# Optimization experiments

Measured on AMD Instinct MI355X. Metric: run time of the kernel, lower is better.

## Reference

```python
import jax, jax.numpy as jnp
import numpy as np

Z_DIM, Y_DIM, X_DIM, N_ACT = 32, 16, 64, 4
TINY_H, HEAD_H = 64, 32
INNER_STEPS, SUP_STEPS = 2, 2
BATCH = 524288


def setup_inputs() -> dict:
    key = jax.random.key(0)
    ks = jax.random.split(key, 12)
    s = lambda k, shp, fan_in: jax.random.normal(k, shp, jnp.float32) * (1.0 / np.sqrt(fan_in))
    return {
        "state": jax.random.normal(ks[0], (BATCH, X_DIM), jnp.float32),
        "prev_action": jax.random.randint(ks[1], (BATCH, 1), 0, N_ACT, jnp.int64),
        "z0": jax.random.normal(ks[2], (1, 1, Z_DIM), jnp.float32) * 0.1,
        # TinyNetwork: Linear(112 -> 64), Linear(64 -> 32); weights stored [out, in]
        "Wt1": s(ks[3], (TINY_H, Z_DIM + X_DIM + Y_DIM), Z_DIM + X_DIM + Y_DIM),
        "bt1": jnp.zeros((TINY_H,), jnp.float32),
        "Wt2": s(ks[4], (Z_DIM, TINY_H), TINY_H),
        "bt2": jnp.zeros((Z_DIM,), jnp.float32),
        # OutputHead: Linear(48 -> 32), Linear(32 -> 4)
        "Wh1": s(ks[5], (HEAD_H, Z_DIM + Y_DIM), Z_DIM + Y_DIM),
        "bh1": jnp.zeros((HEAD_H,), jnp.float32),
        "Wh2": s(ks[6], (N_ACT, HEAD_H), HEAD_H),
        "bh2": jnp.zeros((N_ACT,), jnp.float32),
        # action embedding table [n_actions, y_dim]
        "emb": jax.random.normal(ks[7], (N_ACT, Y_DIM), jnp.float32),
    }


def reference(state, prev_action, z0, Wt1, bt1, Wt2, bt2, Wh1, bh1, Wh2, bh2, emb):
    B = state.shape[0]
    x = state[:, None, :]                      # [B, 1, x_dim]
    y = emb[prev_action]                       # [B, 1, y_dim]
    z = jnp.broadcast_to(z0, (B, 1, Z_DIM))    # [B, 1, z_dim]

    def tiny(z, x, y):
        inp = jnp.concatenate([z, x, y], axis=-1)           # [B,1,112]
        h = jax.nn.relu(inp @ Wt1.T + bt1)                  # [B,1,64]
        return h @ Wt2.T + bt2                              # [B,1,32]

    def head(z, y):
        inp = jnp.concatenate([z, y], axis=-1)              # [B,1,48]
        h = jax.nn.relu(inp @ Wh1.T + bh1)                  # [B,1,32]
        return h @ Wh2.T + bh2                              # [B,1,4]

    logits = None
    for _ in range(SUP_STEPS):
        for _ in range(INNER_STEPS):
            z = tiny(z, x, y)
        logits = head(z, y)
        probs = jax.nn.softmax(logits, axis=-1)             # [B,1,4]
        y = probs @ emb                                     # [B,1,16]
    return logits[:, 0, :]                                  # squeeze seq dim
```

## Files before the change

### kernel.cpp

```cpp
#include <hip/hip_runtime.h>
#include <hip/hip_bf16.h>

typedef __attribute__((ext_vector_type(8))) short bf16x8;
typedef __attribute__((ext_vector_type(4))) float f32x4;

#define MFMA16(A,B,C) __builtin_amdgcn_mfma_f32_16x16x32_bf16((A),(B),(C),0,0,0)

static __device__ __forceinline__ f32x4 ld4(const float* p){
  return *(const f32x4*)p;
}
static __device__ __forceinline__ unsigned pk2(float a, float b){
  unsigned r;
  asm("v_cvt_pk_bf16_f32 %0, %1, %2" : "=v"(r) : "v"(a), "v"(b));
  return r;
}
static __device__ __forceinline__ bf16x8 mk8(float a,float b,float c,float d,
                                             float e,float f,float g,float h){
  union { bf16x8 v; unsigned u[4]; } r;
  r.u[0]=pk2(a,b); r.u[1]=pk2(c,d); r.u[2]=pk2(e,f); r.u[3]=pk2(g,h);
  return r.v;
}
static __device__ __forceinline__ bf16x8 mk8v(f32x4 a, f32x4 b){
  return mk8(a[0],a[1],a[2],a[3],b[0],b[1],b[2],b[3]);
}
static __device__ __forceinline__ bf16x8 mk8r(f32x4 a, f32x4 b){
  return mk8(fmaxf(a[0],0.f),fmaxf(a[1],0.f),fmaxf(a[2],0.f),fmaxf(a[3],0.f),
             fmaxf(b[0],0.f),fmaxf(b[1],0.f),fmaxf(b[2],0.f),fmaxf(b[3],0.f));
}
static __device__ __forceinline__ bf16x8 zero8(){
  bf16x8 v;
  #pragma unroll
  for(int i=0;i<8;++i) v[i]=0;
  return v;
}
static __device__ __forceinline__ void keepa(bf16x8& v){ asm("" : "+a"(v)); }
static __device__ __forceinline__ void keepaf(f32x4& v){ asm("" : "+a"(v)); }

__global__ __launch_bounds__(256, 1) void trm_mfma(
    const float* __restrict__ state, const int* __restrict__ pact,
    const float* __restrict__ z0,
    const float* __restrict__ Wt1, const float* __restrict__ bt1,
    const float* __restrict__ Wt2, const float* __restrict__ bt2,
    const float* __restrict__ Wh1, const float* __restrict__ bh1,
    const float* __restrict__ Wh2, const float* __restrict__ bh2,
    const float* __restrict__ emb, float* __restrict__ out,
    int ntiles, int wstride)
{
  const int lane = threadIdx.x & 63;
  const int wid  = blockIdx.x * (blockDim.x >> 6) + (threadIdx.x >> 6);
  const int r16  = lane & 15;
  const int hi   = lane >> 4;
  const int he   = hi & 1;

  bf16x8 wt1f[4][4];
  #pragma unroll
  for (int m=0;m<4;++m){
    const float* w = Wt1 + (m*16 + r16)*112;
    wt1f[m][0] = mk8v(ld4(w + hi*4),       ld4(w + 16 + hi*4));
    wt1f[m][1] = mk8v(ld4(w + 32 + hi*8),  ld4(w + 36 + hi*8));
    wt1f[m][2] = mk8v(ld4(w + 64 + hi*8),  ld4(w + 68 + hi*8));
    bf16x8 yfrag = mk8v(ld4(w + 96 + he*8), ld4(w + 100 + he*8));
    if (hi >= 2) yfrag = zero8();
    wt1f[m][3] = yfrag;
    keepa(wt1f[m][0]); keepa(wt1f[m][1]); keepa(wt1f[m][2]); keepa(wt1f[m][3]);
  }
  bf16x8 wt2f[2][2];
  #pragma unroll
  for (int m=0;m<2;++m){
    const float* w = Wt2 + (m*16 + r16)*64;
    wt2f[m][0] = mk8v(ld4(w + hi*4),      ld4(w + 16 + hi*4));
    wt2f[m][1] = mk8v(ld4(w + 32 + hi*4), ld4(w + 48 + hi*4));
    keepa(wt2f[m][0]); keepa(wt2f[m][1]);
  }
  bf16x8 wh1f[2][2];
  #pragma unroll
  for (int m=0;m<2;++m){
    const float* w = Wh1 + (m*16 + r16)*48;
    wh1f[m][0] = mk8v(ld4(w + hi*4), ld4(w + 16 + hi*4));
    bf16x8 yfrag = mk8v(ld4(w + 32 + he*8), ld4(w + 36 + he*8));
    if (hi >= 2) yfrag = zero8();
    wh1f[m][1] = yfrag;
    keepa(wh1f[m][0]); keepa(wh1f[m][1]);
  }
  bf16x8 wh2f;
  {
    const float* w = Wh2 + ((r16 < 4) ? r16 : 0)*32;
    bf16x8 t = mk8v(ld4(w + hi*4), ld4(w + 16 + hi*4));
    if (r16 >= 4) t = zero8();
    wh2f = t;
    keepa(wh2f);
  }
  f32x4 bt1r[4], bt2r[2], bh1r[2], bh2r;
  #pragma unroll
  for (int m=0;m<4;++m){ bt1r[m] = ld4(bt1 + m*16 + hi*4); keepaf(bt1r[m]); }
  #pragma unroll
  for (int m=0;m<2;++m){ bt2r[m] = ld4(bt2 + m*16 + hi*4); keepaf(bt2r[m]); }
  #pragma unroll
  for (int m=0;m<2;++m){ bh1r[m] = ld4(bh1 + m*16 + hi*4); keepaf(bh1r[m]); }
  {
    f32x4 t = ld4(bh2);
    float msk = (hi == 0) ? 1.f : 0.f;
    bh2r = t * msk;
    keepaf(bh2r);
  }
  bf16x8 z0f = mk8v(ld4(z0 + hi*4), ld4(z0 + 16 + hi*4));
  keepa(z0f);

  int t = wid;
  f32x4 cx0, cx1, cx2, cx3; int cact;
  {
    const int col = t*16 + r16;
    const float* xr = state + (size_t)col*64;
    cx0 = ld4(xr + hi*8);      cx1 = ld4(xr + hi*8 + 4);
    cx2 = ld4(xr + 32 + hi*8); cx3 = ld4(xr + 36 + hi*8);
    cact = pact[col];
  }

  #pragma unroll 1
  for (; t < ntiles; t += wstride){
    const int col = t*16 + r16;
    bf16x8 xf0 = mk8v(cx0, cx1);
    bf16x8 xf1 = mk8v(cx2, cx3);
    bf16x8 yf;
    {
      const float* er = emb + cact*16 + he*8;
      yf = mk8v(ld4(er), ld4(er + 4));
      if (hi >= 2) yf = zero8();
    }

    const int tn = t + wstride;
    if (tn < ntiles){
      const int coln = tn*16 + r16;
      const float* xrn = state + (size_t)coln*64;
      cx0 = ld4(xrn + hi*8);      cx1 = ld4(xrn + hi*8 + 4);
      cx2 = ld4(xrn + 32 + hi*8); cx3 = ld4(xrn + 36 + hi*8);
      cact = pact[coln];
    }

    bf16x8 zf = z0f;
    f32x4 lgv;

    #pragma unroll
    for (int s=0;s<2;++s){
      #pragma unroll
      for (int itr=0; itr<2; ++itr){
        f32x4 c0 = MFMA16(wt1f[0][0], zf, bt1r[0]);
        f32x4 c1 = MFMA16(wt1f[1][0], zf, bt1r[1]);
        f32x4 c2 = MFMA16(wt1f[2][0], zf, bt1r[2]);
        f32x4 c3 = MFMA16(wt1f[3][0], zf, bt1r[3]);
        c0=MFMA16(wt1f[0][1], xf0, c0); c1=MFMA16(wt1f[1][1], xf0, c1);
        c2=MFMA16(wt1f[2][1], xf0, c2); c3=MFMA16(wt1f[3][1], xf0, c3);
        c0=MFMA16(wt1f[0][2], xf1, c0); c1=MFMA16(wt1f[1][2], xf1, c1);
        c2=MFMA16(wt1f[2][2], xf1, c2); c3=MFMA16(wt1f[3][2], xf1, c3);
        c0=MFMA16(wt1f[0][3], yf,  c0); c1=MFMA16(wt1f[1][3], yf,  c1);
        c2=MFMA16(wt1f[2][3], yf,  c2); c3=MFMA16(wt1f[3][3], yf,  c3);
        bf16x8 h0 = mk8r(c0, c1);
        bf16x8 h1 = mk8r(c2, c3);
        f32x4 d0 = MFMA16(wt2f[0][0], h0, bt2r[0]);
        f32x4 d1 = MFMA16(wt2f[1][0], h0, bt2r[1]);
        d0=MFMA16(wt2f[0][1], h1, d0);
        d1=MFMA16(wt2f[1][1], h1, d1);
        zf = mk8v(d0, d1);
      }
      f32x4 g0 = MFMA16(wh1f[0][0], zf, bh1r[0]);
      f32x4 g1 = MFMA16(wh1f[1][0], zf, bh1r[1]);
      g0=MFMA16(wh1f[0][1], yf, g0);
      g1=MFMA16(wh1f[1][1], yf, g1);
      bf16x8 hh = mk8r(g0, g1);
      f32x4 cl = MFMA16(wh2f, hh, bh2r);
      lgv = cl;
      if (s == 0){
        float l0 = __shfl(cl[0], r16), l1 = __shfl(cl[1], r16);
        float l2 = __shfl(cl[2], r16), l3 = __shfl(cl[3], r16);
        float mx = fmaxf(fmaxf(l0,l1), fmaxf(l2,l3));
        float p0=__expf(l0-mx), p1=__expf(l1-mx);
        float p2=__expf(l2-mx), p3=__expf(l3-mx);
        float inv = 1.f/(p0+p1+p2+p3);
        p0*=inv; p1*=inv; p2*=inv; p3*=inv;
        const float* eb = emb + he*8;
        f32x4 ya = ld4(eb)*p0      + ld4(eb+16)*p1 +
                   ld4(eb+32)*p2   + ld4(eb+48)*p3;
        f32x4 yb = ld4(eb+4)*p0    + ld4(eb+20)*p1 +
                   ld4(eb+36)*p2   + ld4(eb+52)*p3;
        yf = mk8v(ya, yb);
        if (hi >= 2) yf = zero8();
      }
    }
    if (hi == 0) *(f32x4*)(out + (size_t)col*4) = lgv;
  }
}

extern "C" void kernel_launch(void* const* d_in, const int* in_sizes, int n_in,
                              void* d_out, int out_size, void* d_ws, size_t ws_size,
                              hipStream_t stream) {
  const float* state = (const float*)d_in[0];
  const int*   pact  = (const int*)  d_in[1];
  const float* z0    = (const float*)d_in[2];
  const float* Wt1   = (const float*)d_in[3];
  const float* bt1   = (const float*)d_in[4];
  const float* Wt2   = (const float*)d_in[5];
  const float* bt2   = (const float*)d_in[6];
  const float* Wh1   = (const float*)d_in[7];
  const float* bh1   = (const float*)d_in[8];
  const float* Wh2   = (const float*)d_in[9];
  const float* bh2   = (const float*)d_in[10];
  const float* emb   = (const float*)d_in[11];
  float* out = (float*)d_out;

  const int B = in_sizes[0] / 64;
  const int ntiles = B / 16;
  const int blocks = 1024;
  const int wstride = blocks * 4;
  trm_mfma<<<blocks, 256, 0, stream>>>(state, pact, z0, Wt1, bt1, Wt2, bt2,
                                       Wh1, bh1, Wh2, bh2, emb, out,
                                       ntiles, wstride);
}
```

Measured before the change: 63.22 us.

## Fold biases into MFMA via constant-one input lane, stage emb in LDS

Folds bt2 into the downstream biases (bt1' = bt1 + Wt1_z·bt2, bh1' = bh1 + Wh1_z·bt2, z0 shifted by -bt2) and injects those biases through an extra constant-one entry in the padded y fragment. MFMAs can then accumulate from a shared zero register instead of bias registers, which frees registers. The embedding table is staged in shared memory, launch bounds allow two blocks per CU, and the grid is halved. Folding the biases in bf16 adds rounding error, and fewer blocks may reduce latency hiding.

```diff
diff --git a/kernel.cpp b/kernel.cpp
--- a/kernel.cpp
+++ b/kernel.cpp
@@ -33,10 +33,17 @@
   for(int i=0;i<8;++i) v[i]=0;
   return v;
 }
+static __device__ __forceinline__ bf16x8 one8(){
+  bf16x8 v = zero8();
+  v[0] = (short)0x3F80;
+  return v;
+}
 static __device__ __forceinline__ void keepa(bf16x8& v){ asm("" : "+a"(v)); }
 static __device__ __forceinline__ void keepaf(f32x4& v){ asm("" : "+a"(v)); }
-
-__global__ __launch_bounds__(256, 1) void trm_mfma(
+static __device__ __forceinline__ void keepv(bf16x8& v){ asm("" : "+v"(v)); }
+static __device__ __forceinline__ void keepvf(f32x4& v){ asm("" : "+v"(v)); }
+
+__global__ __launch_bounds__(256, 2) void trm_mfma(
     const float* __restrict__ state, const int* __restrict__ pact,
     const float* __restrict__ z0,
     const float* __restrict__ Wt1, const float* __restrict__ bt1,
@@ -46,12 +53,38 @@
     const float* __restrict__ emb, float* __restrict__ out,
     int ntiles, int wstride)
 {
+  __shared__ __align__(16) float ef[64];
   const int lane = threadIdx.x & 63;
   const int wid  = blockIdx.x * (blockDim.x >> 6) + (threadIdx.x >> 6);
   const int r16  = lane & 15;
   const int hi   = lane >> 4;
   const int he   = hi & 1;
 
+  if (threadIdx.x < 64) ef[threadIdx.x] = emb[threadIdx.x];
+  __syncthreads();
+
+  f32x4 b2[8];
+  #pragma unroll
+  for (int q=0;q<8;++q) b2[q] = ld4(bt2 + q*4);
+  float bt1p[4];
+  #pragma unroll
+  for (int m=0;m<4;++m){
+    const float* w = Wt1 + (m*16 + r16)*112;
+    f32x4 s = b2[0]*ld4(w);
+    #pragma unroll
+    for (int q=1;q<8;++q) s += b2[q]*ld4(w + q*4);
+    bt1p[m] = bt1[m*16 + r16] + s[0]+s[1]+s[2]+s[3];
+  }
+  float bh1p[2];
+  #pragma unroll
+  for (int m=0;m<2;++m){
+    const float* w = Wh1 + (m*16 + r16)*48;
+    f32x4 s = b2[0]*ld4(w);
+    #pragma unroll
+    for (int q=1;q<8;++q) s += b2[q]*ld4(w + q*4);
+    bh1p[m] = bh1[m*16 + r16] + s[0]+s[1]+s[2]+s[3];
+  }
+
   bf16x8 wt1f[4][4];
   #pragma unroll
   for (int m=0;m<4;++m){
@@ -59,8 +92,10 @@
     wt1f[m][0] = mk8v(ld4(w + hi*4),       ld4(w + 16 + hi*4));
     wt1f[m][1] = mk8v(ld4(w + 32 + hi*8),  ld4(w + 36 + hi*8));
     wt1f[m][2] = mk8v(ld4(w + 64 + hi*8),  ld4(w + 68 + hi*8));
-    bf16x8 yfrag = mk8v(ld4(w + 96 + he*8), ld4(w + 100 + he*8));
-    if (hi >= 2) yfrag = zero8();
+    bf16x8 yfrag;
+    if (hi < 2)       yfrag = mk8v(ld4(w + 96 + hi*8), ld4(w + 100 + hi*8));
+    else if (hi == 2) yfrag = mk8(bt1p[m],0.f,0.f,0.f,0.f,0.f,0.f,0.f);
+    else              yfrag = zero8();
     wt1f[m][3] = yfrag;
     keepa(wt1f[m][0]); keepa(wt1f[m][1]); keepa(wt1f[m][2]); keepa(wt1f[m][3]);
   }
@@ -77,8 +112,10 @@
   for (int m=0;m<2;++m){
     const float* w = Wh1 + (m*16 + r16)*48;
     wh1f[m][0] = mk8v(ld4(w + hi*4), ld4(w + 16 + hi*4));
-    bf16x8 yfrag = mk8v(ld4(w + 32 + he*8), ld4(w + 36 + he*8));
-    if (hi >= 2) yfrag = zero8();
+    bf16x8 yfrag;
+    if (hi < 2)       yfrag = mk8v(ld4(w + 32 + hi*8), ld4(w + 36 + hi*8));
+    else if (hi == 2) yfrag = mk8(bh1p[m],0.f,0.f,0.f,0.f,0.f,0.f,0.f);
+    else              yfrag = zero8();
     wh1f[m][1] = yfrag;
     keepa(wh1f[m][0]); keepa(wh1f[m][1]);
   }
@@ -90,21 +127,22 @@
     wh2f = t;
     keepa(wh2f);
   }
-  f32x4 bt1r[4], bt2r[2], bh1r[2], bh2r;
-  #pragma unroll
-  for (int m=0;m<4;++m){ bt1r[m] = ld4(bt1 + m*16 + hi*4); keepaf(bt1r[m]); }
-  #pragma unroll
-  for (int m=0;m<2;++m){ bt2r[m] = ld4(bt2 + m*16 + hi*4); keepaf(bt2r[m]); }
-  #pragma unroll
-  for (int m=0;m<2;++m){ bh1r[m] = ld4(bh1 + m*16 + hi*4); keepaf(bh1r[m]); }
+  f32x4 bh2r;
   {
     f32x4 t = ld4(bh2);
     float msk = (hi == 0) ? 1.f : 0.f;
     bh2r = t * msk;
     keepaf(bh2r);
   }
-  bf16x8 z0f = mk8v(ld4(z0 + hi*4), ld4(z0 + 16 + hi*4));
-  keepa(z0f);
+  f32x4 zero4 = {0.f, 0.f, 0.f, 0.f};
+  keepvf(zero4);
+  bf16x8 z0f;
+  {
+    f32x4 za = ld4(z0 + hi*4)      - ld4(bt2 + hi*4);
+    f32x4 zb = ld4(z0 + 16 + hi*4) - ld4(bt2 + 16 + hi*4);
+    z0f = mk8v(za, zb);
+    keepv(z0f);
+  }
 
   int t = wid;
   f32x4 cx0, cx1, cx2, cx3; int cact;
@@ -123,9 +161,10 @@
     bf16x8 xf1 = mk8v(cx2, cx3);
     bf16x8 yf;
     {
-      const float* er = emb + cact*16 + he*8;
+      const float* er = ef + cact*16 + he*8;
       yf = mk8v(ld4(er), ld4(er + 4));
-      if (hi >= 2) yf = zero8();
+      if (hi == 2) yf = one8();
+      if (hi == 3) yf = zero8();
     }
 
     const int tn = t + wstride;
@@ -144,10 +183,10 @@
     for (int s=0;s<2;++s){
       #pragma unroll
       for (int itr=0; itr<2; ++itr){
-        f32x4 c0 = MFMA16(wt1f[0][0], zf, bt1r[0]);
-        f32x4 c1 = MFMA16(wt1f[1][0], zf, bt1r[1]);
-        f32x4 c2 = MFMA16(wt1f[2][0], zf, bt1r[2]);
-        f32x4 c3 = MFMA16(wt1f[3][0], zf, bt1r[3]);
+        f32x4 c0 = MFMA16(wt1f[0][0], zf, zero4);
+        f32x4 c1 = MFMA16(wt1f[1][0], zf, zero4);
+        f32x4 c2 = MFMA16(wt1f[2][0], zf, zero4);
+        f32x4 c3 = MFMA16(wt1f[3][0], zf, zero4);
         c0=MFMA16(wt1f[0][1], xf0, c0); c1=MFMA16(wt1f[1][1], xf0, c1);
         c2=MFMA16(wt1f[2][1], xf0, c2); c3=MFMA16(wt1f[3][1], xf0, c3);
         c0=MFMA16(wt1f[0][2], xf1, c0); c1=MFMA16(wt1f[1][2], xf1, c1);
@@ -156,14 +195,14 @@
         c2=MFMA16(wt1f[2][3], yf,  c2); c3=MFMA16(wt1f[3][3], yf,  c3);
         bf16x8 h0 = mk8r(c0, c1);
         bf16x8 h1 = mk8r(c2, c3);
-        f32x4 d0 = MFMA16(wt2f[0][0], h0, bt2r[0]);
-        f32x4 d1 = MFMA16(wt2f[1][0], h0, bt2r[1]);
+        f32x4 d0 = MFMA16(wt2f[0][0], h0, zero4);
+        f32x4 d1 = MFMA16(wt2f[1][0], h0, zero4);
         d0=MFMA16(wt2f[0][1], h1, d0);
         d1=MFMA16(wt2f[1][1], h1, d1);
         zf = mk8v(d0, d1);
       }
-      f32x4 g0 = MFMA16(wh1f[0][0], zf, bh1r[0]);
-      f32x4 g1 = MFMA16(wh1f[1][0], zf, bh1r[1]);
+      f32x4 g0 = MFMA16(wh1f[0][0], zf, zero4);
+      f32x4 g1 = MFMA16(wh1f[1][0], zf, zero4);
       g0=MFMA16(wh1f[0][1], yf, g0);
       g1=MFMA16(wh1f[1][1], yf, g1);
       bf16x8 hh = mk8r(g0, g1);
@@ -177,13 +216,14 @@
         float p2=__expf(l2-mx), p3=__expf(l3-mx);
         float inv = 1.f/(p0+p1+p2+p3);
         p0*=inv; p1*=inv; p2*=inv; p3*=inv;
-        const float* eb = emb + he*8;
+        const float* eb = ef + he*8;
         f32x4 ya = ld4(eb)*p0      + ld4(eb+16)*p1 +
                    ld4(eb+32)*p2   + ld4(eb+48)*p3;
         f32x4 yb = ld4(eb+4)*p0    + ld4(eb+20)*p1 +
                    ld4(eb+36)*p2   + ld4(eb+52)*p3;
         yf = mk8v(ya, yb);
-        if (hi >= 2) yf = zero8();
+        if (hi == 2) yf = one8();
+        if (hi == 3) yf = zero8();
       }
     }
     if (hi == 0) *(f32x4*)(out + (size_t)col*4) = lgv;
@@ -209,7 +249,7 @@
 
   const int B = in_sizes[0] / 64;
   const int ntiles = B / 16;
-  const int blocks = 1024;
+  const int blocks = 512;
   const int wstride = blocks * 4;
   trm_mfma<<<blocks, 256, 0, stream>>>(state, pact, z0, Wt1, bt1, Wt2, bt2,
                                        Wh1, bh1, Wh2, bh2, emb, out,
```

New measurement: 64.59 us. 2.2% more time.
